# Performance work log

Hardware: AMD Instinct MI355X
Metric: run time of the kernel (lower is better)

Reference implementation:

```python
import jax, jax.numpy as jnp
import numpy as np

B, H, E = 1024, 2048, 1024

def _xavier(key, shape):
    # torch xavier_normal_ on [1, out, in]: std = sqrt(2/(fan_in+fan_out)) over last two dims
    fan_out, fan_in = shape[-2], shape[-1]
    std = (2.0 / (fan_in + fan_out)) ** 0.5
    return jax.random.normal(key, shape, jnp.float32) * std

def setup_inputs() -> dict:
    key = jax.random.key(0)
    ks = jax.random.split(key, 17)
    inp = {
        'x': jax.random.normal(ks[0], (B, E, 1), jnp.float32),
        'c': jax.random.normal(ks[1], (B, H, 1), jnp.float32),
        'h': jax.random.normal(ks[2], (B, H, 1), jnp.float32),
        'W_xi': _xavier(ks[3], (1, H, E)), 'W_hi': _xavier(ks[4], (1, H, H)), 'B_i': _xavier(ks[5], (1, H, 1)),
        'W_xg': _xavier(ks[6], (1, H, E)), 'W_hg': _xavier(ks[7], (1, H, H)), 'B_g': _xavier(ks[8], (1, H, 1)),
        'W_xf': _xavier(ks[9], (1, H, E)), 'W_hf': _xavier(ks[10], (1, H, H)), 'B_f': _xavier(ks[11], (1, H, 1)),
        'W_xo': _xavier(ks[12], (1, H, E)), 'W_ho': _xavier(ks[13], (1, H, H)), 'B_o': _xavier(ks[14], (1, H, 1)),
        'W_hy': _xavier(ks[15], (1, E, H)), 'B_y': _xavier(ks[16], (1, E, 1)),
    }
    return inp

def reference(x, c, h, W_xi, W_hi, B_i, W_xg, W_hg, B_g, W_xf, W_hf, B_f, W_xo, W_ho, B_o, W_hy, B_y):
    # jnp.matmul broadcasts the leading batch dim: [1,H,E] @ [B,E,1] -> [B,H,1]
    i = jax.nn.sigmoid(jnp.matmul(W_xi, x) + jnp.matmul(W_hi, h) + B_i)
    g = jnp.tanh(jnp.matmul(W_xg, x) + jnp.matmul(W_hg, h) + B_g)
    f = jax.nn.sigmoid(jnp.matmul(W_xf, x) + jnp.matmul(W_hf, h) + B_f)
    c_new = f * c + i * g
    o = jax.nn.sigmoid(jnp.matmul(W_xo, x) + jnp.matmul(W_ho, h) + B_o)
    h_new = o * c_new  # NOTE: source uses o*c (no tanh), faithful to original
    y = jnp.tanh(jnp.matmul(W_hy, h_new) + B_y)
    return (y, c_new, h_new)
```

## Files before the change

### kernel.cpp

```cpp
#include <hip/hip_runtime.h>

#define B_SZ 1024
#define H_SZ 2048
#define E_SZ 1024

typedef float  f32x4 __attribute__((ext_vector_type(4)));
typedef short  s16x8 __attribute__((ext_vector_type(8)));

__device__ __forceinline__ unsigned short f2bf(float f) {
    unsigned u = __float_as_uint(f);
    u = u + 0x7fffu + ((u >> 16) & 1u);
    return (unsigned short)(u >> 16);
}
__device__ __forceinline__ float bf2f(unsigned short s) {
    return __uint_as_float(((unsigned)s) << 16);
}
__device__ __forceinline__ float sigm(float v) {
    return 1.0f / (1.0f + __expf(-v));
}

__device__ __forceinline__ void gll(const unsigned short* g, unsigned short* l) {
    __builtin_amdgcn_global_load_lds(
        (const __attribute__((address_space(1))) unsigned int*)g,
        (__attribute__((address_space(3))) unsigned int*)l, 16, 0, 0);
}

struct CastArgs {
    const float*    src[11];
    unsigned short* dst[11];
    int             n[11];
};

__global__ __launch_bounds__(256) void cast_kernel(CastArgs a) {
    const int arr = blockIdx.y;
    const int n = a.n[arr];
    const float* __restrict__ s = a.src[arr];
    unsigned short* __restrict__ d = a.dst[arr];
    const int stride = gridDim.x * 256 * 4;
    for (int i = (blockIdx.x * 256 + threadIdx.x) * 4; i < n; i += stride) {
        float4 v = *(const float4*)(s + i);
        ushort4 o;
        o.x = f2bf(v.x); o.y = f2bf(v.y); o.z = f2bf(v.z); o.w = f2bf(v.w);
        *(ushort4*)(d + i) = o;
    }
}

__device__ __forceinline__ void gemm_accum64(
    const unsigned short* __restrict__ A,
    const unsigned short* __restrict__ W,
    int ld, int kLen, int m0, int n0,
    unsigned short* lA, unsigned short* lB,
    f32x4 acc[4][4], int t)
{
    const int lane = t & 63;
    const int w    = t >> 6;
    const int wr   = (w >> 1) << 6;
    const int wc   = (w & 1) << 6;
    const int lr   = lane & 15;
    const int q4   = lane >> 4;

    const int srow = t >> 3;
    const int scol = ((t & 7) ^ (srow & 7)) << 3;
    const unsigned short* gA = A + (size_t)(m0 + srow) * ld + scol;
    const unsigned short* gB = W + (size_t)(n0 + srow) * ld + scol;
    const size_t st32 = (size_t)32 * ld;

    const int cb0 = ((q4    ) ^ (lr & 7)) << 3;
    const int cb1 = ((4 + q4) ^ (lr & 7)) << 3;

    for (int k0 = 0; k0 < kLen; k0 += 64) {
#pragma unroll
        for (int p = 0; p < 4; ++p)
            gll(gA + k0 + p * st32, lA + (t + 256 * p) * 8);
#pragma unroll
        for (int p = 0; p < 4; ++p)
            gll(gB + k0 + p * st32, lB + (t + 256 * p) * 8);
        __syncthreads();

#pragma unroll
        for (int ks = 0; ks < 2; ++ks) {
            const int cb = ks ? cb1 : cb0;
            s16x8 af[4], bfr[4];
#pragma unroll
            for (int i = 0; i < 4; ++i)
                af[i] = *(const s16x8*)(lA + (wr + i * 16 + lr) * 64 + cb);
#pragma unroll
            for (int j = 0; j < 4; ++j)
                bfr[j] = *(const s16x8*)(lB + (wc + j * 16 + lr) * 64 + cb);
#pragma unroll
            for (int i = 0; i < 4; ++i)
#pragma unroll
                for (int j = 0; j < 4; ++j)
                    acc[i][j] = __builtin_amdgcn_mfma_f32_16x16x32_bf16(
                        af[i], bfr[j], acc[i][j], 0, 0, 0);
        }
        __syncthreads();
    }
}

__global__ __launch_bounds__(256) void gates_kernel(
    const unsigned short* __restrict__ Xb,
    const unsigned short* __restrict__ Hb,
    const unsigned short* __restrict__ Wxb,
    const unsigned short* __restrict__ Whb,
    const float* __restrict__ bi, const float* __restrict__ bg,
    const float* __restrict__ bff, const float* __restrict__ bo,
    unsigned short* __restrict__ Z)
{
    __shared__ unsigned short lA[128 * 64];
    __shared__ unsigned short lB[128 * 64];
    const int t   = threadIdx.x;
    const int b   = blockIdx.x;
    const int xcd = b & 7;
    const int i_  = b >> 3;
    const int nt  = xcd * 8 + (i_ >> 3);
    const int m0  = (i_ & 7) * 128;
    const int q   = nt >> 4;
    const int n0  = (nt & 15) * 128;

    f32x4 acc[4][4] = {};
    gemm_accum64(Xb, Wxb + (size_t)q * H_SZ * E_SZ, E_SZ, E_SZ, m0, n0, lA, lB, acc, t);
    gemm_accum64(Hb, Whb + (size_t)q * H_SZ * H_SZ, H_SZ, H_SZ, m0, n0, lA, lB, acc, t);

    const float* bias = (q == 0) ? bi : (q == 1) ? bg : (q == 2) ? bff : bo;
    const int lane = t & 63, w = t >> 6;
    const int wr = (w >> 1) << 6, wc = (w & 1) << 6;
    const int lr = lane & 15, rq = (lane >> 4) << 2;
    unsigned short* Zq = Z + (size_t)q * B_SZ * H_SZ;
#pragma unroll
    for (int i = 0; i < 4; ++i) {
#pragma unroll
        for (int j = 0; j < 4; ++j) {
            const int n = n0 + wc + j * 16 + lr;
            const float bv = bias[n];
#pragma unroll
            for (int r = 0; r < 4; ++r) {
                const int m = m0 + wr + i * 16 + rq + r;
                const float v = acc[i][j][r] + bv;
                const float a = (q == 1) ? tanhf(v) : sigm(v);
                Zq[(size_t)m * H_SZ + n] = f2bf(a);
            }
        }
    }
}

__global__ __launch_bounds__(256) void cell_kernel(
    const unsigned short* __restrict__ Z, const float* __restrict__ c,
    float* __restrict__ c_out, float* __restrict__ h_out,
    unsigned short* __restrict__ HnB)
{
    const size_t BH = (size_t)B_SZ * H_SZ;
    const int idx = (blockIdx.x * 256 + threadIdx.x) * 4;
    ushort4 iu = *(const ushort4*)(Z + idx);
    ushort4 gu = *(const ushort4*)(Z + BH + idx);
    ushort4 fu = *(const ushort4*)(Z + 2 * BH + idx);
    ushort4 ou = *(const ushort4*)(Z + 3 * BH + idx);
    float4 cv = *(const float4*)(c + idx);

    float cn[4], hn[4];
    cn[0] = bf2f(fu.x) * cv.x + bf2f(iu.x) * bf2f(gu.x);
    cn[1] = bf2f(fu.y) * cv.y + bf2f(iu.y) * bf2f(gu.y);
    cn[2] = bf2f(fu.z) * cv.z + bf2f(iu.z) * bf2f(gu.z);
    cn[3] = bf2f(fu.w) * cv.w + bf2f(iu.w) * bf2f(gu.w);
    hn[0] = bf2f(ou.x) * cn[0];
    hn[1] = bf2f(ou.y) * cn[1];
    hn[2] = bf2f(ou.z) * cn[2];
    hn[3] = bf2f(ou.w) * cn[3];

    *(float4*)(c_out + idx) = make_float4(cn[0], cn[1], cn[2], cn[3]);
    *(float4*)(h_out + idx) = make_float4(hn[0], hn[1], hn[2], hn[3]);
    ushort4 hb;
    hb.x = f2bf(hn[0]); hb.y = f2bf(hn[1]); hb.z = f2bf(hn[2]); hb.w = f2bf(hn[3]);
    *(ushort4*)(HnB + idx) = hb;
}

__global__ __launch_bounds__(256) void y_split_kernel(
    const unsigned short* __restrict__ Hn,
    const unsigned short* __restrict__ Wy,
    float* __restrict__ part)
{
    __shared__ unsigned short lA[128 * 64];
    __shared__ unsigned short lB[128 * 64];
    const int t   = threadIdx.x;
    const int b   = blockIdx.x;
    const int xcd = b & 7;
    const int i_  = b >> 3;
    const int ns  = xcd * 4 + (i_ >> 3);
    const int m0  = (i_ & 7) * 128;
    const int n0  = (ns >> 2) * 128;
    const int s   = ns & 3;

    f32x4 acc[4][4] = {};
    gemm_accum64(Hn + s * 512, Wy + s * 512, H_SZ, 512, m0, n0, lA, lB, acc, t);

    const int lane = t & 63, w = t >> 6;
    const int wr = (w >> 1) << 6, wc = (w & 1) << 6;
    const int lr = lane & 15, rq = (lane >> 4) << 2;
    float* P = part + (size_t)s * B_SZ * E_SZ;
#pragma unroll
    for (int i = 0; i < 4; ++i) {
#pragma unroll
        for (int j = 0; j < 4; ++j) {
            const int n = n0 + wc + j * 16 + lr;
#pragma unroll
            for (int r = 0; r < 4; ++r) {
                const int m = m0 + wr + i * 16 + rq + r;
                P[(size_t)m * E_SZ + n] = acc[i][j][r];
            }
        }
    }
}

__global__ __launch_bounds__(256) void y_reduce_kernel(
    const float* __restrict__ part, const float* __restrict__ by,
    float* __restrict__ yout)
{
    const size_t BE = (size_t)B_SZ * E_SZ;
    const int idx = (blockIdx.x * 256 + threadIdx.x) * 4;
    float4 a = *(const float4*)(part + idx);
    float4 b2 = *(const float4*)(part + BE + idx);
    float4 c2 = *(const float4*)(part + 2 * BE + idx);
    float4 d2 = *(const float4*)(part + 3 * BE + idx);
    const int col = idx & (E_SZ - 1);
    float4 bv = *(const float4*)(by + col);
    float4 o;
    o.x = tanhf(a.x + b2.x + c2.x + d2.x + bv.x);
    o.y = tanhf(a.y + b2.y + c2.y + d2.y + bv.y);
    o.z = tanhf(a.z + b2.z + c2.z + d2.z + bv.z);
    o.w = tanhf(a.w + b2.w + c2.w + d2.w + bv.w);
    *(float4*)(yout + idx) = o;
}

extern "C" void kernel_launch(void* const* d_in, const int* in_sizes, int n_in,
                              void* d_out, int out_size, void* d_ws, size_t ws_size,
                              hipStream_t stream) {
    const float* x   = (const float*)d_in[0];
    const float* c   = (const float*)d_in[1];
    const float* h   = (const float*)d_in[2];
    const float* Wxi = (const float*)d_in[3];
    const float* Whi = (const float*)d_in[4];
    const float* Bi  = (const float*)d_in[5];
    const float* Wxg = (const float*)d_in[6];
    const float* Whg = (const float*)d_in[7];
    const float* Bg  = (const float*)d_in[8];
    const float* Wxf = (const float*)d_in[9];
    const float* Whf = (const float*)d_in[10];
    const float* Bf  = (const float*)d_in[11];
    const float* Wxo = (const float*)d_in[12];
    const float* Who = (const float*)d_in[13];
    const float* Bo  = (const float*)d_in[14];
    const float* Why = (const float*)d_in[15];
    const float* By  = (const float*)d_in[16];

    const size_t BE = (size_t)B_SZ * E_SZ, BH = (size_t)B_SZ * H_SZ;
    const size_t HE = (size_t)H_SZ * E_SZ, HH = (size_t)H_SZ * H_SZ;
    const size_t EH = (size_t)E_SZ * H_SZ;

    unsigned short* ws   = (unsigned short*)d_ws;
    unsigned short* Xb   = ws;
    unsigned short* Hb   = Xb + BE;
    unsigned short* Wxb  = Hb + BH;
    unsigned short* Whb  = Wxb + 4 * HE;
    unsigned short* Whyb = Whb + 4 * HH;
    unsigned short* Z    = Whyb + EH;
    unsigned short* HnB  = Z + 4 * BH;

    CastArgs ca;
    ca.src[0]  = x;   ca.dst[0]  = Xb;           ca.n[0]  = (int)BE;
    ca.src[1]  = h;   ca.dst[1]  = Hb;           ca.n[1]  = (int)BH;
    ca.src[2]  = Wxi; ca.dst[2]  = Wxb;          ca.n[2]  = (int)HE;
    ca.src[3]  = Wxg; ca.dst[3]  = Wxb + HE;     ca.n[3]  = (int)HE;
    ca.src[4]  = Wxf; ca.dst[4]  = Wxb + 2 * HE; ca.n[4]  = (int)HE;
    ca.src[5]  = Wxo; ca.dst[5]  = Wxb + 3 * HE; ca.n[5]  = (int)HE;
    ca.src[6]  = Whi; ca.dst[6]  = Whb;          ca.n[6]  = (int)HH;
    ca.src[7]  = Whg; ca.dst[7]  = Whb + HH;     ca.n[7]  = (int)HH;
    ca.src[8]  = Whf; ca.dst[8]  = Whb + 2 * HH; ca.n[8]  = (int)HH;
    ca.src[9]  = Who; ca.dst[9]  = Whb + 3 * HH; ca.n[9]  = (int)HH;
    ca.src[10] = Why; ca.dst[10] = Whyb;         ca.n[10] = (int)EH;

    hipLaunchKernelGGL(cast_kernel, dim3(1024, 11), dim3(256), 0, stream, ca);
    hipLaunchKernelGGL(gates_kernel, dim3(512), dim3(256), 0, stream,
                       Xb, Hb, Wxb, Whb, Bi, Bg, Bf, Bo, Z);

    float* y_out = (float*)d_out;
    float* c_out = y_out + BE;
    float* h_out = c_out + BH;
    hipLaunchKernelGGL(cell_kernel, dim3((unsigned)(BH / 1024)), dim3(256), 0, stream,
                       Z, c, c_out, h_out, HnB);

    float* ypart = (float*)Z;
    hipLaunchKernelGGL(y_split_kernel, dim3(256), dim3(256), 0, stream,
                       HnB, Whyb, ypart);
    hipLaunchKernelGGL(y_reduce_kernel, dim3((unsigned)(BE / 1024)), dim3(256), 0, stream,
                       ypart, By, y_out);
}
```

Baseline: 267.0 us.

## Pre-swizzle bf16 operands into MFMA fragment order and load directly to registers

The cast kernel now writes the bf16 copies of inputs and weights in a tiled layout that matches the MFMA fragment order. The gates and y GEMMs can then read fragments straight from global memory into registers with a double-buffered software pipeline, with no LDS staging and no barriers. The cell kernel writes h_new in the same swizzled layout for the y GEMM. This removes LDS traffic and synchronisation, but every operand is now re-read from global memory or L2 by each wave, since there is no sharing across waves through LDS.

```diff
diff --git a/kernel.cpp b/kernel.cpp
--- a/kernel.cpp
+++ b/kernel.cpp
@@ -19,112 +19,102 @@
     return 1.0f / (1.0f + __expf(-v));
 }
 
-__device__ __forceinline__ void gll(const unsigned short* g, unsigned short* l) {
-    __builtin_amdgcn_global_load_lds(
-        (const __attribute__((address_space(1))) unsigned int*)g,
-        (__attribute__((address_space(3))) unsigned int*)l, 16, 0, 0);
-}
-
-struct CastArgs {
+struct SwArgs {
     const float*    src[11];
     unsigned short* dst[11];
-    int             n[11];
+    int             log2K[11];
+    int             nthr[11];
 };
 
-__global__ __launch_bounds__(256) void cast_kernel(CastArgs a) {
+__global__ __launch_bounds__(256) void swcast_kernel(SwArgs a) {
     const int arr = blockIdx.y;
-    const int n = a.n[arr];
-    const float* __restrict__ s = a.src[arr];
-    unsigned short* __restrict__ d = a.dst[arr];
-    const int stride = gridDim.x * 256 * 4;
-    for (int i = (blockIdx.x * 256 + threadIdx.x) * 4; i < n; i += stride) {
-        float4 v = *(const float4*)(s + i);
-        ushort4 o;
-        o.x = f2bf(v.x); o.y = f2bf(v.y); o.z = f2bf(v.z); o.w = f2bf(v.w);
-        *(ushort4*)(d + i) = o;
-    }
-}
-
-__device__ __forceinline__ void gemm_accum64(
-    const unsigned short* __restrict__ A,
-    const unsigned short* __restrict__ W,
-    int ld, int kLen, int m0, int n0,
-    unsigned short* lA, unsigned short* lB,
-    f32x4 acc[4][4], int t)
-{
+    const int t = blockIdx.x * 256 + threadIdx.x;
+    if (t >= a.nthr[arr]) return;
+    const int lg   = a.log2K[arr];
     const int lane = t & 63;
-    const int w    = t >> 6;
-    const int wr   = (w >> 1) << 6;
-    const int wc   = (w & 1) << 6;
-    const int lr   = lane & 15;
-    const int q4   = lane >> 4;
-
-    const int srow = t >> 3;
-    const int scol = ((t & 7) ^ (srow & 7)) << 3;
-    const unsigned short* gA = A + (size_t)(m0 + srow) * ld + scol;
-    const unsigned short* gB = W + (size_t)(n0 + srow) * ld + scol;
-    const size_t st32 = (size_t)32 * ld;
-
-    const int cb0 = ((q4    ) ^ (lr & 7)) << 3;
-    const int cb1 = ((4 + q4) ^ (lr & 7)) << 3;
-
-    for (int k0 = 0; k0 < kLen; k0 += 64) {
-#pragma unroll
-        for (int p = 0; p < 4; ++p)
-            gll(gA + k0 + p * st32, lA + (t + 256 * p) * 8);
-#pragma unroll
-        for (int p = 0; p < 4; ++p)
-            gll(gB + k0 + p * st32, lB + (t + 256 * p) * 8);
-        __syncthreads();
-
-#pragma unroll
-        for (int ks = 0; ks < 2; ++ks) {
-            const int cb = ks ? cb1 : cb0;
-            s16x8 af[4], bfr[4];
-#pragma unroll
-            for (int i = 0; i < 4; ++i)
-                af[i] = *(const s16x8*)(lA + (wr + i * 16 + lr) * 64 + cb);
-#pragma unroll
-            for (int j = 0; j < 4; ++j)
-                bfr[j] = *(const s16x8*)(lB + (wc + j * 16 + lr) * 64 + cb);
-#pragma unroll
-            for (int i = 0; i < 4; ++i)
-#pragma unroll
-                for (int j = 0; j < 4; ++j)
-                    acc[i][j] = __builtin_amdgcn_mfma_f32_16x16x32_bf16(
-                        af[i], bfr[j], acc[i][j], 0, 0, 0);
-        }
-        __syncthreads();
-    }
-}
+    const int u    = t >> 6;
+    const int hj   = u & 7;
+    const int v    = u >> 3;
+    const int k32m = (1 << (lg - 5)) - 1;
+    const int ks   = v & k32m;
+    const int nt   = v >> (lg - 5);
+    const int row  = (nt << 7) + ((hj >> 2) << 6) + ((hj & 3) << 4) + (lane & 15);
+    const int k    = (ks << 5) + ((lane >> 4) << 3);
+    const float* s = a.src[arr] + ((size_t)row << lg) + k;
+    float4 v0 = *(const float4*)s;
+    float4 v1 = *(const float4*)(s + 4);
+    s16x8 o;
+    o[0] = (short)f2bf(v0.x); o[1] = (short)f2bf(v0.y);
+    o[2] = (short)f2bf(v0.z); o[3] = (short)f2bf(v0.w);
+    o[4] = (short)f2bf(v1.x); o[5] = (short)f2bf(v1.y);
+    o[6] = (short)f2bf(v1.z); o[7] = (short)f2bf(v1.w);
+    *(s16x8*)(a.dst[arr] + (size_t)t * 8) = o;
+}
+
+#define LDF(dst, base, ks)                                                  \
+    _Pragma("unroll") for (int _i = 0; _i < 4; ++_i)                        \
+        dst[_i] = *(const s16x8*)((base) + (ks) * 4096 + _i * 512);
+
+#define MF(aa, bb)                                                          \
+    _Pragma("unroll") for (int _i = 0; _i < 4; ++_i)                        \
+    _Pragma("unroll") for (int _j = 0; _j < 4; ++_j)                        \
+        acc[_i][_j] = __builtin_amdgcn_mfma_f32_16x16x32_bf16(              \
+            aa[_i], bb[_j], acc[_i][_j], 0, 0, 0);
 
 __global__ __launch_bounds__(256) void gates_kernel(
-    const unsigned short* __restrict__ Xb,
-    const unsigned short* __restrict__ Hb,
-    const unsigned short* __restrict__ Wxb,
-    const unsigned short* __restrict__ Whb,
+    const unsigned short* __restrict__ Xsw,
+    const unsigned short* __restrict__ Hsw,
+    const unsigned short* __restrict__ Wxsw,
+    const unsigned short* __restrict__ Whsw,
     const float* __restrict__ bi, const float* __restrict__ bg,
     const float* __restrict__ bff, const float* __restrict__ bo,
     unsigned short* __restrict__ Z)
 {
-    __shared__ unsigned short lA[128 * 64];
-    __shared__ unsigned short lB[128 * 64];
     const int t   = threadIdx.x;
     const int b   = blockIdx.x;
     const int xcd = b & 7;
     const int i_  = b >> 3;
     const int nt  = xcd * 8 + (i_ >> 3);
-    const int m0  = (i_ & 7) * 128;
+    const int mt  = i_ & 7;
     const int q   = nt >> 4;
-    const int n0  = (nt & 15) * 128;
+    const int n0t = nt & 15;
+    const int lane = t & 63, w = t >> 6;
+    const int hm = w >> 1, hn = w & 1;
+
+    const unsigned short* ax = Xsw + (size_t)(mt * 256 + hm * 4) * 512 + lane * 8;
+    const unsigned short* bx = Wxsw + (size_t)q * H_SZ * E_SZ
+                             + (size_t)(n0t * 256 + hn * 4) * 512 + lane * 8;
+    const unsigned short* ah = Hsw + (size_t)(mt * 512 + hm * 4) * 512 + lane * 8;
+    const unsigned short* bh = Whsw + (size_t)q * H_SZ * H_SZ
+                             + (size_t)(n0t * 512 + hn * 4) * 512 + lane * 8;
 
     f32x4 acc[4][4] = {};
-    gemm_accum64(Xb, Wxb + (size_t)q * H_SZ * E_SZ, E_SZ, E_SZ, m0, n0, lA, lB, acc, t);
-    gemm_accum64(Hb, Whb + (size_t)q * H_SZ * H_SZ, H_SZ, H_SZ, m0, n0, lA, lB, acc, t);
+    s16x8 a0[4], b0[4], a1[4], b1[4];
+
+    LDF(a0, ax, 0); LDF(b0, bx, 0);
+    for (int ks = 0; ks < 30; ks += 2) {
+        LDF(a1, ax, ks + 1); LDF(b1, bx, ks + 1);
+        MF(a0, b0);
+        LDF(a0, ax, ks + 2); LDF(b0, bx, ks + 2);
+        MF(a1, b1);
+    }
+    LDF(a1, ax, 31); LDF(b1, bx, 31);
+    MF(a0, b0);
+    LDF(a0, ah, 0); LDF(b0, bh, 0);
+    MF(a1, b1);
+    for (int ks = 0; ks < 62; ks += 2) {
+        LDF(a1, ah, ks + 1); LDF(b1, bh, ks + 1);
+        MF(a0, b0);
+        LDF(a0, ah, ks + 2); LDF(b0, bh, ks + 2);
+        MF(a1, b1);
+    }
+    LDF(a1, ah, 63); LDF(b1, bh, 63);
+    MF(a0, b0);
+    MF(a1, b1);
 
     const float* bias = (q == 0) ? bi : (q == 1) ? bg : (q == 2) ? bff : bo;
-    const int lane = t & 63, w = t >> 6;
-    const int wr = (w >> 1) << 6, wc = (w & 1) << 6;
+    const int m0 = mt * 128, n0 = n0t * 128;
+    const int wr = hm << 6, wc = hn << 6;
     const int lr = lane & 15, rq = (lane >> 4) << 2;
     unsigned short* Zq = Z + (size_t)q * B_SZ * H_SZ;
 #pragma unroll
@@ -147,54 +137,80 @@
 __global__ __launch_bounds__(256) void cell_kernel(
     const unsigned short* __restrict__ Z, const float* __restrict__ c,
     float* __restrict__ c_out, float* __restrict__ h_out,
-    unsigned short* __restrict__ HnB)
+    unsigned short* __restrict__ Hnsw)
 {
     const size_t BH = (size_t)B_SZ * H_SZ;
-    const int idx = (blockIdx.x * 256 + threadIdx.x) * 4;
-    ushort4 iu = *(const ushort4*)(Z + idx);
-    ushort4 gu = *(const ushort4*)(Z + BH + idx);
-    ushort4 fu = *(const ushort4*)(Z + 2 * BH + idx);
-    ushort4 ou = *(const ushort4*)(Z + 3 * BH + idx);
-    float4 cv = *(const float4*)(c + idx);
-
-    float cn[4], hn[4];
-    cn[0] = bf2f(fu.x) * cv.x + bf2f(iu.x) * bf2f(gu.x);
-    cn[1] = bf2f(fu.y) * cv.y + bf2f(iu.y) * bf2f(gu.y);
-    cn[2] = bf2f(fu.z) * cv.z + bf2f(iu.z) * bf2f(gu.z);
-    cn[3] = bf2f(fu.w) * cv.w + bf2f(iu.w) * bf2f(gu.w);
-    hn[0] = bf2f(ou.x) * cn[0];
-    hn[1] = bf2f(ou.y) * cn[1];
-    hn[2] = bf2f(ou.z) * cn[2];
-    hn[3] = bf2f(ou.w) * cn[3];
-
-    *(float4*)(c_out + idx) = make_float4(cn[0], cn[1], cn[2], cn[3]);
-    *(float4*)(h_out + idx) = make_float4(hn[0], hn[1], hn[2], hn[3]);
-    ushort4 hb;
-    hb.x = f2bf(hn[0]); hb.y = f2bf(hn[1]); hb.z = f2bf(hn[2]); hb.w = f2bf(hn[3]);
-    *(ushort4*)(HnB + idx) = hb;
+    const int t8 = blockIdx.x * 256 + threadIdx.x;
+    const size_t base = (size_t)t8 * 8;
+
+    s16x8 iu = *(const s16x8*)(Z + base);
+    s16x8 gu = *(const s16x8*)(Z + BH + base);
+    s16x8 fu = *(const s16x8*)(Z + 2 * BH + base);
+    s16x8 ou = *(const s16x8*)(Z + 3 * BH + base);
+    float4 c0 = *(const float4*)(c + base);
+    float4 c1 = *(const float4*)(c + base + 4);
+    const float cv[8] = {c0.x, c0.y, c0.z, c0.w, c1.x, c1.y, c1.z, c1.w};
+
+    float cn[8], hn[8];
+#pragma unroll
+    for (int e = 0; e < 8; ++e) {
+        cn[e] = bf2f((unsigned short)fu[e]) * cv[e]
+              + bf2f((unsigned short)iu[e]) * bf2f((unsigned short)gu[e]);
+        hn[e] = bf2f((unsigned short)ou[e]) * cn[e];
+    }
+    *(float4*)(c_out + base)     = make_float4(cn[0], cn[1], cn[2], cn[3]);
+    *(float4*)(c_out + base + 4) = make_float4(cn[4], cn[5], cn[6], cn[7]);
+    *(float4*)(h_out + base)     = make_float4(hn[0], hn[1], hn[2], hn[3]);
+    *(float4*)(h_out + base + 4) = make_float4(hn[4], hn[5], hn[6], hn[7]);
+
+    const int m  = (int)(base >> 11);
+    const int hk = (int)(base & 2047);
+    const int mt = m >> 7, half = (m >> 6) & 1, ii = (m >> 4) & 3, lr = m & 15;
+    const int ks = hk >> 5, kq3 = (hk >> 3) & 3;
+    const int lane2 = (kq3 << 4) | lr;
+    const size_t toff = ((((size_t)mt * 64 + ks) * 8 + half * 4 + ii) * 64 + lane2) * 8;
+    s16x8 hb;
+#pragma unroll
+    for (int e = 0; e < 8; ++e) hb[e] = (short)f2bf(hn[e]);
+    *(s16x8*)(Hnsw + toff) = hb;
 }
 
 __global__ __launch_bounds__(256) void y_split_kernel(
-    const unsigned short* __restrict__ Hn,
-    const unsigned short* __restrict__ Wy,
+    const unsigned short* __restrict__ Hnsw,
+    const unsigned short* __restrict__ Whysw,
     float* __restrict__ part)
 {
-    __shared__ unsigned short lA[128 * 64];
-    __shared__ unsigned short lB[128 * 64];
     const int t   = threadIdx.x;
     const int b   = blockIdx.x;
     const int xcd = b & 7;
     const int i_  = b >> 3;
     const int ns  = xcd * 4 + (i_ >> 3);
-    const int m0  = (i_ & 7) * 128;
-    const int n0  = (ns >> 2) * 128;
+    const int mt  = i_ & 7;
+    const int n0t = ns >> 2;
     const int s   = ns & 3;
+    const int lane = t & 63, w = t >> 6;
+    const int hm = w >> 1, hn = w & 1;
+
+    const unsigned short* ay = Hnsw
+        + (size_t)((mt * 64 + s * 16) * 8 + hm * 4) * 512 + lane * 8;
+    const unsigned short* by = Whysw
+        + (size_t)((n0t * 64 + s * 16) * 8 + hn * 4) * 512 + lane * 8;
 
     f32x4 acc[4][4] = {};
-    gemm_accum64(Hn + s * 512, Wy + s * 512, H_SZ, 512, m0, n0, lA, lB, acc, t);
-
-    const int lane = t & 63, w = t >> 6;
-    const int wr = (w >> 1) << 6, wc = (w & 1) << 6;
+    s16x8 a0[4], b0[4], a1[4], b1[4];
+    LDF(a0, ay, 0); LDF(b0, by, 0);
+    for (int ks = 0; ks < 14; ks += 2) {
+        LDF(a1, ay, ks + 1); LDF(b1, by, ks + 1);
+        MF(a0, b0);
+        LDF(a0, ay, ks + 2); LDF(b0, by, ks + 2);
+        MF(a1, b1);
+    }
+    LDF(a1, ay, 15); LDF(b1, by, 15);
+    MF(a0, b0);
+    MF(a1, b1);
+
+    const int m0 = mt * 128, n0 = n0t * 128;
+    const int wr = hm << 6, wc = hn << 6;
     const int lr = lane & 15, rq = (lane >> 4) << 2;
     float* P = part + (size_t)s * B_SZ * E_SZ;
 #pragma unroll
@@ -256,41 +272,41 @@
     const size_t HE = (size_t)H_SZ * E_SZ, HH = (size_t)H_SZ * H_SZ;
     const size_t EH = (size_t)E_SZ * H_SZ;
 
-    unsigned short* ws   = (unsigned short*)d_ws;
-    unsigned short* Xb   = ws;
-    unsigned short* Hb   = Xb + BE;
-    unsigned short* Wxb  = Hb + BH;
-    unsigned short* Whb  = Wxb + 4 * HE;
-    unsigned short* Whyb = Whb + 4 * HH;
-    unsigned short* Z    = Whyb + EH;
-    unsigned short* HnB  = Z + 4 * BH;
-
-    CastArgs ca;
-    ca.src[0]  = x;   ca.dst[0]  = Xb;           ca.n[0]  = (int)BE;
-    ca.src[1]  = h;   ca.dst[1]  = Hb;           ca.n[1]  = (int)BH;
-    ca.src[2]  = Wxi; ca.dst[2]  = Wxb;          ca.n[2]  = (int)HE;
-    ca.src[3]  = Wxg; ca.dst[3]  = Wxb + HE;     ca.n[3]  = (int)HE;
-    ca.src[4]  = Wxf; ca.dst[4]  = Wxb + 2 * HE; ca.n[4]  = (int)HE;
-    ca.src[5]  = Wxo; ca.dst[5]  = Wxb + 3 * HE; ca.n[5]  = (int)HE;
-    ca.src[6]  = Whi; ca.dst[6]  = Whb;          ca.n[6]  = (int)HH;
-    ca.src[7]  = Whg; ca.dst[7]  = Whb + HH;     ca.n[7]  = (int)HH;
-    ca.src[8]  = Whf; ca.dst[8]  = Whb + 2 * HH; ca.n[8]  = (int)HH;
-    ca.src[9]  = Who; ca.dst[9]  = Whb + 3 * HH; ca.n[9]  = (int)HH;
-    ca.src[10] = Why; ca.dst[10] = Whyb;         ca.n[10] = (int)EH;
-
-    hipLaunchKernelGGL(cast_kernel, dim3(1024, 11), dim3(256), 0, stream, ca);
+    unsigned short* ws    = (unsigned short*)d_ws;
+    unsigned short* Xsw   = ws;
+    unsigned short* Hsw   = Xsw + BE;
+    unsigned short* Wxsw  = Hsw + BH;
+    unsigned short* Whsw  = Wxsw + 4 * HE;
+    unsigned short* Whysw = Whsw + 4 * HH;
+    unsigned short* Z     = Whysw + EH;
+    unsigned short* Hnsw  = Z + 4 * BH;
+
+    SwArgs sa;
+    sa.src[0]  = x;   sa.dst[0]  = Xsw;          sa.log2K[0]  = 10; sa.nthr[0]  = (int)(BE / 8);
+    sa.src[1]  = h;   sa.dst[1]  = Hsw;          sa.log2K[1]  = 11; sa.nthr[1]  = (int)(BH / 8);
+    sa.src[2]  = Wxi; sa.dst[2]  = Wxsw;         sa.log2K[2]  = 10; sa.nthr[2]  = (int)(HE / 8);
+    sa.src[3]  = Wxg; sa.dst[3]  = Wxsw + HE;    sa.log2K[3]  = 10; sa.nthr[3]  = (int)(HE / 8);
+    sa.src[4]  = Wxf; sa.dst[4]  = Wxsw + 2*HE;  sa.log2K[4]  = 10; sa.nthr[4]  = (int)(HE / 8);
+    sa.src[5]  = Wxo; sa.dst[5]  = Wxsw + 3*HE;  sa.log2K[5]  = 10; sa.nthr[5]  = (int)(HE / 8);
+    sa.src[6]  = Whi; sa.dst[6]  = Whsw;         sa.log2K[6]  = 11; sa.nthr[6]  = (int)(HH / 8);
+    sa.src[7]  = Whg; sa.dst[7]  = Whsw + HH;    sa.log2K[7]  = 11; sa.nthr[7]  = (int)(HH / 8);
+    sa.src[8]  = Whf; sa.dst[8]  = Whsw + 2*HH;  sa.log2K[8]  = 11; sa.nthr[8]  = (int)(HH / 8);
+    sa.src[9]  = Who; sa.dst[9]  = Whsw + 3*HH;  sa.log2K[9]  = 11; sa.nthr[9]  = (int)(HH / 8);
+    sa.src[10] = Why; sa.dst[10] = Whysw;        sa.log2K[10] = 11; sa.nthr[10] = (int)(EH / 8);
+
+    hipLaunchKernelGGL(swcast_kernel, dim3(2048, 11), dim3(256), 0, stream, sa);
     hipLaunchKernelGGL(gates_kernel, dim3(512), dim3(256), 0, stream,
-                       Xb, Hb, Wxb, Whb, Bi, Bg, Bf, Bo, Z);
+                       Xsw, Hsw, Wxsw, Whsw, Bi, Bg, Bf, Bo, Z);
 
     float* y_out = (float*)d_out;
     float* c_out = y_out + BE;
     float* h_out = c_out + BH;
-    hipLaunchKernelGGL(cell_kernel, dim3((unsigned)(BH / 1024)), dim3(256), 0, stream,
-                       Z, c, c_out, h_out, HnB);
+    hipLaunchKernelGGL(cell_kernel, dim3((unsigned)(BH / 2048)), dim3(256), 0, stream,
+                       Z, c, c_out, h_out, Hnsw);
 
     float* ypart = (float*)Z;
     hipLaunchKernelGGL(y_split_kernel, dim3(256), dim3(256), 0, stream,
-                       HnB, Whyb, ypart);
+                       Hnsw, Whysw, ypart);
     hipLaunchKernelGGL(y_reduce_kernel, dim3((unsigned)(BE / 1024)), dim3(256), 0, stream,
                        ypart, By, y_out);
 }
```

Measured after the change: 281.5 us. 5.4% more time.

## Fuse fp32-to-bf16 weight conversion into GEMM tile loads, drop weight cast pass

Applied to the files above, without the earlier changes.

The separate cast pass that converted all weight matrices to bf16 is removed. The GEMM loaders now read fp32 weights directly, truncate them to bf16 with byte permutes, and store the packed values into the swizzled LDS tile. This avoids writing and re-reading the bf16 weight copy. In exchange, each weight tile is fetched at twice the bytes and is re-read by every M tile, the loads go through registers instead of direct-to-LDS, and rounding changes from round-to-nearest to truncation.

```diff
diff --git a/kernel.cpp b/kernel.cpp
--- a/kernel.cpp
+++ b/kernel.cpp
@@ -18,7 +18,6 @@
 __device__ __forceinline__ float sigm(float v) {
     return 1.0f / (1.0f + __expf(-v));
 }
-
 __device__ __forceinline__ void gll(const unsigned short* g, unsigned short* l) {
     __builtin_amdgcn_global_load_lds(
         (const __attribute__((address_space(1))) unsigned int*)g,
@@ -26,9 +25,9 @@
 }
 
 struct CastArgs {
-    const float*    src[11];
-    unsigned short* dst[11];
-    int             n[11];
+    const float*    src[2];
+    unsigned short* dst[2];
+    int             n[2];
 };
 
 __global__ __launch_bounds__(256) void cast_kernel(CastArgs a) {
@@ -45,10 +44,10 @@
     }
 }
 
-__device__ __forceinline__ void gemm_accum64(
+__device__ __forceinline__ void gemm_f32w(
     const unsigned short* __restrict__ A,
-    const unsigned short* __restrict__ W,
-    int ld, int kLen, int m0, int n0,
+    const float* __restrict__ W,
+    int ldA, int ldB, int kLen, int m0, int n0,
     unsigned short* lA, unsigned short* lB,
     f32x4 acc[4][4], int t)
 {
@@ -60,10 +59,13 @@
     const int q4   = lane >> 4;
 
     const int srow = t >> 3;
-    const int scol = ((t & 7) ^ (srow & 7)) << 3;
-    const unsigned short* gA = A + (size_t)(m0 + srow) * ld + scol;
-    const unsigned short* gB = W + (size_t)(n0 + srow) * ld + scol;
-    const size_t st32 = (size_t)32 * ld;
+    const int swc8 = (t & 7) ^ (srow & 7);
+    const int scol = swc8 << 3;
+    const unsigned short* gA = A + (size_t)(m0 + srow) * ldA + scol;
+    const float*          gB = W + (size_t)(n0 + srow) * ldB + ((t & 7) << 3);
+    const size_t stA = (size_t)32 * ldA;
+    const size_t stB = (size_t)32 * ldB;
+    unsigned short* lBw = lB + srow * 64 + scol;
 
     const int cb0 = ((q4    ) ^ (lr & 7)) << 3;
     const int cb1 = ((4 + q4) ^ (lr & 7)) << 3;
@@ -71,10 +73,27 @@
     for (int k0 = 0; k0 < kLen; k0 += 64) {
 #pragma unroll
         for (int p = 0; p < 4; ++p)
-            gll(gA + k0 + p * st32, lA + (t + 256 * p) * 8);
-#pragma unroll
-        for (int p = 0; p < 4; ++p)
-            gll(gB + k0 + p * st32, lB + (t + 256 * p) * 8);
+            gll(gA + k0 + p * stA, lA + (t + 256 * p) * 8);
+        float4 f0[4], f1[4];
+#pragma unroll
+        for (int p = 0; p < 4; ++p) {
+            const float* s = gB + k0 + p * stB;
+            f0[p] = *(const float4*)s;
+            f1[p] = *(const float4*)(s + 4);
+        }
+#pragma unroll
+        for (int p = 0; p < 4; ++p) {
+            uint4 pk;
+            pk.x = __builtin_amdgcn_perm(__float_as_uint(f0[p].y),
+                        __float_as_uint(f0[p].x), 0x07060302u);
+            pk.y = __builtin_amdgcn_perm(__float_as_uint(f0[p].w),
+                        __float_as_uint(f0[p].z), 0x07060302u);
+            pk.z = __builtin_amdgcn_perm(__float_as_uint(f1[p].y),
+                        __float_as_uint(f1[p].x), 0x07060302u);
+            pk.w = __builtin_amdgcn_perm(__float_as_uint(f1[p].w),
+                        __float_as_uint(f1[p].z), 0x07060302u);
+            *(uint4*)(lBw + p * 32 * 64) = pk;
+        }
         __syncthreads();
 
 #pragma unroll
@@ -101,8 +120,10 @@
 __global__ __launch_bounds__(256) void gates_kernel(
     const unsigned short* __restrict__ Xb,
     const unsigned short* __restrict__ Hb,
-    const unsigned short* __restrict__ Wxb,
-    const unsigned short* __restrict__ Whb,
+    const float* __restrict__ Wxi, const float* __restrict__ Wxg,
+    const float* __restrict__ Wxf, const float* __restrict__ Wxo,
+    const float* __restrict__ Whi, const float* __restrict__ Whg,
+    const float* __restrict__ Whf, const float* __restrict__ Who,
     const float* __restrict__ bi, const float* __restrict__ bg,
     const float* __restrict__ bff, const float* __restrict__ bo,
     unsigned short* __restrict__ Z)
@@ -118,9 +139,12 @@
     const int q   = nt >> 4;
     const int n0  = (nt & 15) * 128;
 
+    const float* Wxq = (q == 0) ? Wxi : (q == 1) ? Wxg : (q == 2) ? Wxf : Wxo;
+    const float* Whq = (q == 0) ? Whi : (q == 1) ? Whg : (q == 2) ? Whf : Who;
+
     f32x4 acc[4][4] = {};
-    gemm_accum64(Xb, Wxb + (size_t)q * H_SZ * E_SZ, E_SZ, E_SZ, m0, n0, lA, lB, acc, t);
-    gemm_accum64(Hb, Whb + (size_t)q * H_SZ * H_SZ, H_SZ, H_SZ, m0, n0, lA, lB, acc, t);
+    gemm_f32w(Xb, Wxq, E_SZ, E_SZ, E_SZ, m0, n0, lA, lB, acc, t);
+    gemm_f32w(Hb, Whq, H_SZ, H_SZ, H_SZ, m0, n0, lA, lB, acc, t);
 
     const float* bias = (q == 0) ? bi : (q == 1) ? bg : (q == 2) ? bff : bo;
     const int lane = t & 63, w = t >> 6;
@@ -176,7 +200,7 @@
 
 __global__ __launch_bounds__(256) void y_split_kernel(
     const unsigned short* __restrict__ Hn,
-    const unsigned short* __restrict__ Wy,
+    const float* __restrict__ Wy,
     float* __restrict__ part)
 {
     __shared__ unsigned short lA[128 * 64];
@@ -191,7 +215,7 @@
     const int s   = ns & 3;
 
     f32x4 acc[4][4] = {};
-    gemm_accum64(Hn + s * 512, Wy + s * 512, H_SZ, 512, m0, n0, lA, lB, acc, t);
+    gemm_f32w(Hn + s * 512, Wy + s * 512, H_SZ, H_SZ, 512, m0, n0, lA, lB, acc, t);
 
     const int lane = t & 63, w = t >> 6;
     const int wr = (w >> 1) << 6, wc = (w & 1) << 6;
@@ -253,34 +277,21 @@
     const float* By  = (const float*)d_in[16];
 
     const size_t BE = (size_t)B_SZ * E_SZ, BH = (size_t)B_SZ * H_SZ;
-    const size_t HE = (size_t)H_SZ * E_SZ, HH = (size_t)H_SZ * H_SZ;
-    const size_t EH = (size_t)E_SZ * H_SZ;
-
-    unsigned short* ws   = (unsigned short*)d_ws;
-    unsigned short* Xb   = ws;
-    unsigned short* Hb   = Xb + BE;
-    unsigned short* Wxb  = Hb + BH;
-    unsigned short* Whb  = Wxb + 4 * HE;
-    unsigned short* Whyb = Whb + 4 * HH;
-    unsigned short* Z    = Whyb + EH;
-    unsigned short* HnB  = Z + 4 * BH;
+
+    unsigned short* ws  = (unsigned short*)d_ws;
+    unsigned short* Xb  = ws;
+    unsigned short* Hb  = Xb + BE;
+    unsigned short* Z   = Hb + BH;
+    unsigned short* HnB = Z + 4 * BH;
 
     CastArgs ca;
-    ca.src[0]  = x;   ca.dst[0]  = Xb;           ca.n[0]  = (int)BE;
-    ca.src[1]  = h;   ca.dst[1]  = Hb;           ca.n[1]  = (int)BH;
-    ca.src[2]  = Wxi; ca.dst[2]  = Wxb;          ca.n[2]  = (int)HE;
-    ca.src[3]  = Wxg; ca.dst[3]  = Wxb + HE;     ca.n[3]  = (int)HE;
-    ca.src[4]  = Wxf; ca.dst[4]  = Wxb + 2 * HE; ca.n[4]  = (int)HE;
-    ca.src[5]  = Wxo; ca.dst[5]  = Wxb + 3 * HE; ca.n[5]  = (int)HE;
-    ca.src[6]  = Whi; ca.dst[6]  = Whb;          ca.n[6]  = (int)HH;
-    ca.src[7]  = Whg; ca.dst[7]  = Whb + HH;     ca.n[7]  = (int)HH;
-    ca.src[8]  = Whf; ca.dst[8]  = Whb + 2 * HH; ca.n[8]  = (int)HH;
-    ca.src[9]  = Who; ca.dst[9]  = Whb + 3 * HH; ca.n[9]  = (int)HH;
-    ca.src[10] = Why; ca.dst[10] = Whyb;         ca.n[10] = (int)EH;
-
-    hipLaunchKernelGGL(cast_kernel, dim3(1024, 11), dim3(256), 0, stream, ca);
+    ca.src[0] = x; ca.dst[0] = Xb; ca.n[0] = (int)BE;
+    ca.src[1] = h; ca.dst[1] = Hb; ca.n[1] = (int)BH;
+
+    hipLaunchKernelGGL(cast_kernel, dim3(1024, 2), dim3(256), 0, stream, ca);
     hipLaunchKernelGGL(gates_kernel, dim3(512), dim3(256), 0, stream,
-                       Xb, Hb, Wxb, Whb, Bi, Bg, Bf, Bo, Z);
+                       Xb, Hb, Wxi, Wxg, Wxf, Wxo, Whi, Whg, Whf, Who,
+                       Bi, Bg, Bf, Bo, Z);
 
     float* y_out = (float*)d_out;
     float* c_out = y_out + BE;
@@ -290,7 +301,7 @@
 
     float* ypart = (float*)Z;
     hipLaunchKernelGGL(y_split_kernel, dim3(256), dim3(256), 0, stream,
-                       HnB, Whyb, ypart);
+                       HnB, Why, ypart);
     hipLaunchKernelGGL(y_reduce_kernel, dim3((unsigned)(BE / 1024)), dim3(256), 0, stream,
                        ypart, By, y_out);
 }
```

Result: slower. 283.4 us (+6.2%).
